# Optimization experiments

Hardware: AMD Instinct MI355X
Metric: run time of the kernel (lower is better)

The kernel has to match this reference:

```python
import jax, jax.numpy as jnp
import numpy as np


def _fft_upsample2(x):
    """Ideal (sinc) 2x upsample via FFT zero-padding, with Nyquist-bin splitting.
    x: [B, C, H, W] real -> [B, C, 2H, 2W] real."""
    H, W = x.shape[-2], x.shape[-1]
    hh, hw = H // 2, W // 2
    # shifted spectrum: index i along length-H axis <-> frequency i - H/2
    X = jnp.fft.fftshift(jnp.fft.fft2(x), axes=(-2, -1))
    Y = jnp.zeros(x.shape[:-2] + (2 * H, 2 * W), X.dtype)
    Y = Y.at[..., hh:hh + H, hw:hw + W].set(X)
    # split Nyquist row -H/2 (index hh) into +/-H/2 (indices hh and hh+H), each half
    Y = Y.at[..., hh, :].multiply(0.5)
    Y = Y.at[..., hh + H, :].set(Y[..., hh, :])
    # same for Nyquist column
    Y = Y.at[..., :, hw].multiply(0.5)
    Y = Y.at[..., :, hw + W].set(Y[..., :, hw])
    y = jnp.fft.ifft2(jnp.fft.ifftshift(Y, axes=(-2, -1))).real
    return (y * 4.0).astype(x.dtype)  # up**2 amplitude correction


def _lpf_rect_1d(N, cutoff):
    # create_lpf_rect from alias_free_convnets: ideal rect LPF in frequency
    cl = int(N * cutoff) // 2
    ch = N - cl
    rect = np.ones(N, dtype=np.float32)
    rect[cl + 1:ch] = 0.0
    if N % 4 == 0:  # half-weight on the exact cutoff (Nyquist-of-subband) bins
        rect[cl] = 0.5
        rect[ch] = 0.5
    return rect


def _lpf_rfft(x, cutoff=0.5):
    """Ideal low-pass via rfft2 with rectangular separable mask."""
    H, W = x.shape[-2], x.shape[-1]
    rect_h = _lpf_rect_1d(H, cutoff)
    rect_w = _lpf_rect_1d(W, cutoff)
    mask = jnp.asarray(rect_h[:, None] * rect_w[None, :W // 2 + 1])
    X = jnp.fft.rfft2(x) * mask
    return jnp.fft.irfft2(X, s=(H, W)).astype(x.dtype)


def setup_inputs() -> dict:
    key = jax.random.key(0)
    x = jax.random.normal(key, (8, 256, 64, 64), dtype=jnp.float32)
    return {"x": x}


def reference(x):
    u = _fft_upsample2(x)          # [B, C, 2H, 2W]
    a = jax.nn.silu(u)
    f = _lpf_rfft(a, cutoff=0.5)   # [B, C, 2H, 2W]
    return f[:, :, ::2, ::2]       # [B, C, H, W]
```

## Files before the change

kernel.cpp:

```cpp
#include <hip/hip_runtime.h>
#include <math.h>

#define TPB 256

typedef _Float16 f16x8 __attribute__((ext_vector_type(8)));
typedef float    f32x4 __attribute__((ext_vector_type(4)));

#define MFMA16(A, B, C) __builtin_amdgcn_mfma_f32_16x16x32_f16((A), (B), (C), 0, 0, 0)


__device__ __forceinline__ void store4h(_Float16* p, float a0, float a1, float a2, float a3) {
  float2 q;
  q.x = __builtin_bit_cast(float, __builtin_amdgcn_cvt_pkrtz(a0, a1));
  q.y = __builtin_bit_cast(float, __builtin_amdgcn_cvt_pkrtz(a2, a3));
  *(float2*)p = q;
}

__global__ __launch_bounds__(TPB, 3) void warped_mfma(const float* __restrict__ xin,
                                                      float* __restrict__ outp, int nimg) {
  constexpr int SA = 72;
  constexpr int SB = 136;
  constexpr int SZ = 68;

  __shared__ __attribute__((aligned(16))) unsigned char bufA[128 * SB * 2];
  __shared__ __attribute__((aligned(16))) unsigned char bufB[128 * SA * 2];
  __shared__ float k1d[128];

  _Float16* const buf0 = (_Float16*)bufA;
  _Float16* const buf2 = (_Float16*)bufA;
  float*    const buf4 = (float*)bufA;
  _Float16* const buf1 = (_Float16*)bufB;
  _Float16* const buf3 = (_Float16*)bufB;

  const int tid = threadIdx.x;
  const int lane = tid & 63;
  const int w  = tid >> 6;
  const int wk = w >> 1;
  const int wd = w & 1;
  const int lq = lane >> 4;
  const int ln = lane & 15;

  if (tid < 128) {
    const int d = tid;
    float s = 1.0f + ((d & 1) ? 0.0f : ((d & 2) ? -1.0f : 1.0f));
    for (int f = 1; f <= 31; ++f) {
      int r = (f * d) & 127;
      s += 2.0f * __cosf((float)r * 0.04908738521234052f );
    }
    k1d[d] = s * (1.0f / 64.0f);
  }
  __syncthreads();

  f16x8 AK[4][2];
#pragma unroll
  for (int t = 0; t < 4; ++t)
#pragma unroll
    for (int ks = 0; ks < 2; ++ks) {
      const int a = (wk * 4 + t) * 16 + ln;
      f16x8 f;
#pragma unroll
      for (int j = 0; j < 8; ++j) {
        int k = ks * 32 + lq * 8 + j;
        f[j] = (_Float16)k1d[(a - 2 * k) & 127];
      }
      AK[t][ks] = f;
    }
  f16x8 BT[2][4];
#pragma unroll
  for (int t = 0; t < 2; ++t)
#pragma unroll
    for (int ks = 0; ks < 4; ++ks) {
      const int c = (wk * 2 + t) * 16 + ln;
      f16x8 f;
#pragma unroll
      for (int j = 0; j < 8; ++j) {
        int k = ks * 32 + lq * 8 + j;
        f[j] = (_Float16)k1d[(k - 2 * c) & 127];
      }
      BT[t][ks] = f;
    }

  const f32x4 vzero = {0.0f, 0.0f, 0.0f, 0.0f};

  for (int img = blockIdx.x; img < nimg; img += gridDim.x) {
    const float* __restrict__ x = xin + (size_t)img * 4096;
    float* __restrict__ out     = outp + (size_t)img * 4096;

#pragma unroll
    for (int rep = 0; rep < 4; ++rep) {
      int idx = rep * 256 + tid;
      float4 v = ((const float4*)x)[idx];
      int i = idx >> 4, j0 = (idx & 15) << 2;
      store4h(buf0 + i * SA + j0, v.x, v.y, v.z, v.w);
    }
    __syncthreads();

    {
      f32x4 acc[2][4];
#pragma unroll
      for (int mtl = 0; mtl < 2; ++mtl)
#pragma unroll
        for (int ntl = 0; ntl < 4; ++ntl) acc[mtl][ntl] = vzero;
#pragma unroll
      for (int ks = 0; ks < 2; ++ks) {
        f16x8 Ad[2];
#pragma unroll
        for (int mtl = 0; mtl < 2; ++mtl)
          Ad[mtl] = *(const f16x8*)(buf0 + ((wd * 2 + mtl) * 16 + ln) * SA + ks * 32 + lq * 8);
#pragma unroll
        for (int mtl = 0; mtl < 2; ++mtl)
#pragma unroll
          for (int ntl = 0; ntl < 4; ++ntl)
            acc[mtl][ntl] = MFMA16(Ad[mtl], AK[ntl][ks], acc[mtl][ntl]);
      }
#pragma unroll
      for (int mtl = 0; mtl < 2; ++mtl)
#pragma unroll
        for (int ntl = 0; ntl < 4; ++ntl) {
          int n0 = (wk * 4 + ntl) * 16, m0 = (wd * 2 + mtl) * 16;
          f32x4 a = acc[mtl][ntl];
          store4h(buf1 + (n0 + ln) * SA + m0 + lq * 4, a[0], a[1], a[2], a[3]);
        }
    }
    __syncthreads();

#pragma unroll
    for (int nh = 0; nh < 2; ++nh) {
      f32x4 acc[4][2];
#pragma unroll
      for (int mtl = 0; mtl < 4; ++mtl)
#pragma unroll
        for (int ntl = 0; ntl < 2; ++ntl) acc[mtl][ntl] = vzero;
#pragma unroll
      for (int ks = 0; ks < 2; ++ks) {
        f16x8 Bd[2];
#pragma unroll
        for (int ntl = 0; ntl < 2; ++ntl)
          Bd[ntl] =
              *(const f16x8*)(buf1 + ((wd * 4 + nh * 2 + ntl) * 16 + ln) * SA + ks * 32 + lq * 8);
#pragma unroll
        for (int mtl = 0; mtl < 4; ++mtl)
#pragma unroll
          for (int ntl = 0; ntl < 2; ++ntl)
            acc[mtl][ntl] = MFMA16(AK[mtl][ks], Bd[ntl], acc[mtl][ntl]);
      }
#pragma unroll
      for (int mtl = 0; mtl < 4; ++mtl)
#pragma unroll
        for (int ntl = 0; ntl < 2; ++ntl) {
          int n0 = (wd * 4 + nh * 2 + ntl) * 16, m0 = (wk * 4 + mtl) * 16;
          float s[4];
#pragma unroll
          for (int r = 0; r < 4; ++r) {
            float u = acc[mtl][ntl][r];
            s[r] = u * __builtin_amdgcn_rcpf(1.0f + __expf(-u));
          }
          store4h(buf2 + (n0 + ln) * SB + m0 + lq * 4, s[0], s[1], s[2], s[3]);
        }
    }
    __syncthreads();

    {
      f32x4 acc[4][2];
#pragma unroll
      for (int mtl = 0; mtl < 4; ++mtl)
#pragma unroll
        for (int ntl = 0; ntl < 2; ++ntl) acc[mtl][ntl] = vzero;
#pragma unroll
      for (int ks = 0; ks < 4; ++ks) {
        f16x8 Ad[4];
#pragma unroll
        for (int mtl = 0; mtl < 4; ++mtl)
          Ad[mtl] = *(const f16x8*)(buf2 + ((wd * 4 + mtl) * 16 + ln) * SB + ks * 32 + lq * 8);
#pragma unroll
        for (int mtl = 0; mtl < 4; ++mtl)
#pragma unroll
          for (int ntl = 0; ntl < 2; ++ntl)
            acc[mtl][ntl] = MFMA16(Ad[mtl], BT[ntl][ks], acc[mtl][ntl]);
      }
#pragma unroll
      for (int mtl = 0; mtl < 4; ++mtl)
#pragma unroll
        for (int ntl = 0; ntl < 2; ++ntl) {
          int n0 = (wk * 2 + ntl) * 16, m0 = (wd * 4 + mtl) * 16;
          f32x4 a = acc[mtl][ntl];
          store4h(buf3 + (n0 + ln) * SB + m0 + lq * 4, a[0], a[1], a[2], a[3]);
        }
    }
    __syncthreads();

    {
      f32x4 acc[2][2];
#pragma unroll
      for (int mtl = 0; mtl < 2; ++mtl)
#pragma unroll
        for (int ntl = 0; ntl < 2; ++ntl) acc[mtl][ntl] = vzero;
#pragma unroll
      for (int ks = 0; ks < 4; ++ks) {
        f16x8 Ad[2];
#pragma unroll
        for (int mtl = 0; mtl < 2; ++mtl)
          Ad[mtl] = *(const f16x8*)(buf3 + ((wd * 2 + mtl) * 16 + ln) * SB + ks * 32 + lq * 8);
#pragma unroll
        for (int mtl = 0; mtl < 2; ++mtl)
#pragma unroll
          for (int ntl = 0; ntl < 2; ++ntl)
            acc[mtl][ntl] = MFMA16(Ad[mtl], BT[ntl][ks], acc[mtl][ntl]);
      }
#pragma unroll
      for (int mtl = 0; mtl < 2; ++mtl)
#pragma unroll
        for (int ntl = 0; ntl < 2; ++ntl) {
          int n0 = (wk * 2 + ntl) * 16, m0 = (wd * 2 + mtl) * 16;
          f32x4 o = acc[mtl][ntl];
          o[0] *= 0.25f; o[1] *= 0.25f; o[2] *= 0.25f; o[3] *= 0.25f;
          *(f32x4*)(buf4 + (n0 + ln) * SZ + m0 + lq * 4) = o;
        }
    }
    __syncthreads();

#pragma unroll
    for (int rep = 0; rep < 4; ++rep) {
      int a = (tid >> 4) + rep * 16;
      int b0 = (tid & 15) << 2;
      float4 o;
      o.x = buf4[(b0 + 0) * SZ + a];
      o.y = buf4[(b0 + 1) * SZ + a];
      o.z = buf4[(b0 + 2) * SZ + a];
      o.w = buf4[(b0 + 3) * SZ + a];
      ((float4*)out)[(a * 64 + b0) >> 2] = o;
    }
    __syncthreads();
  }
}

extern "C" void kernel_launch(void* const* d_in, const int* in_sizes, int n_in,
                              void* d_out, int out_size, void* d_ws, size_t ws_size,
                              hipStream_t stream) {
  const float* x = (const float*)d_in[0];
  float* out = (float*)d_out;
  const int nimg = in_sizes[0] / 4096;
  const int grid = (nimg + 1) / 2;
  warped_mfma<<<dim3(grid), dim3(TPB), 0, stream>>>(x, out, nimg);
}
```

Baseline: 96.54 us.

## Swizzle LDS tiles instead of padding and store output directly from MFMA accumulators

Replaces the padded LDS row strides with XOR-swizzled addressing for the 64- and 128-wide fp16 tiles, which avoids bank conflicts without padding and shrinks the LDS footprint. It also drops the final fp32 LDS transpose stage and its two barriers, writing the scaled accumulators straight to global memory. The cost is scalar, less coalesced global stores (16 contiguous floats per row segment) in place of float4 stores.

New measurement: 116.1 us. 20.3% more time.

```diff
diff --git a/kernel.cpp b/kernel.cpp
--- a/kernel.cpp
+++ b/kernel.cpp
@@ -8,6 +8,13 @@
 
 #define MFMA16(A, B, C) __builtin_amdgcn_mfma_f32_16x16x32_f16((A), (B), (C), 0, 0, 0)
 
+
+__device__ __forceinline__ int sw64(int r, int c) {
+  return (r << 6) + (c & 7) + ((((c >> 3) ^ r) & 7) << 3);
+}
+__device__ __forceinline__ int sw128(int r, int c) {
+  return (r << 7) + (c & 7) + ((((c >> 3) ^ (r & 7))) << 3);
+}
 
 __device__ __forceinline__ void store4h(_Float16* p, float a0, float a1, float a2, float a3) {
   float2 q;
@@ -18,19 +25,14 @@
 
 __global__ __launch_bounds__(TPB, 3) void warped_mfma(const float* __restrict__ xin,
                                                       float* __restrict__ outp, int nimg) {
-  constexpr int SA = 72;
-  constexpr int SB = 136;
-  constexpr int SZ = 68;
-
-  __shared__ __attribute__((aligned(16))) unsigned char bufA[128 * SB * 2];
-  __shared__ __attribute__((aligned(16))) unsigned char bufB[128 * SA * 2];
+  __shared__ __attribute__((aligned(16))) _Float16 bufA[128 * 128];
+  __shared__ __attribute__((aligned(16))) _Float16 bufB[128 * 64];
   __shared__ float k1d[128];
 
-  _Float16* const buf0 = (_Float16*)bufA;
-  _Float16* const buf2 = (_Float16*)bufA;
-  float*    const buf4 = (float*)bufA;
-  _Float16* const buf1 = (_Float16*)bufB;
-  _Float16* const buf3 = (_Float16*)bufB;
+  _Float16* const buf0 = bufA;
+  _Float16* const buf2 = bufA;
+  _Float16* const buf1 = bufB;
+  _Float16* const buf3 = bufB;
 
   const int tid = threadIdx.x;
   const int lane = tid & 63;
@@ -91,7 +93,7 @@
       int idx = rep * 256 + tid;
       float4 v = ((const float4*)x)[idx];
       int i = idx >> 4, j0 = (idx & 15) << 2;
-      store4h(buf0 + i * SA + j0, v.x, v.y, v.z, v.w);
+      store4h(buf0 + sw64(i, j0), v.x, v.y, v.z, v.w);
     }
     __syncthreads();
 
@@ -106,7 +108,7 @@
         f16x8 Ad[2];
 #pragma unroll
         for (int mtl = 0; mtl < 2; ++mtl)
-          Ad[mtl] = *(const f16x8*)(buf0 + ((wd * 2 + mtl) * 16 + ln) * SA + ks * 32 + lq * 8);
+          Ad[mtl] = *(const f16x8*)(buf0 + sw64((wd * 2 + mtl) * 16 + ln, ks * 32 + lq * 8));
 #pragma unroll
         for (int mtl = 0; mtl < 2; ++mtl)
 #pragma unroll
@@ -119,7 +121,7 @@
         for (int ntl = 0; ntl < 4; ++ntl) {
           int n0 = (wk * 4 + ntl) * 16, m0 = (wd * 2 + mtl) * 16;
           f32x4 a = acc[mtl][ntl];
-          store4h(buf1 + (n0 + ln) * SA + m0 + lq * 4, a[0], a[1], a[2], a[3]);
+          store4h(buf1 + sw64(n0 + ln, m0 + lq * 4), a[0], a[1], a[2], a[3]);
         }
     }
     __syncthreads();
@@ -136,8 +138,8 @@
         f16x8 Bd[2];
 #pragma unroll
         for (int ntl = 0; ntl < 2; ++ntl)
-          Bd[ntl] =
-              *(const f16x8*)(buf1 + ((wd * 4 + nh * 2 + ntl) * 16 + ln) * SA + ks * 32 + lq * 8);
+          Bd[ntl] = *(const f16x8*)(buf1 +
+                                    sw64((wd * 4 + nh * 2 + ntl) * 16 + ln, ks * 32 + lq * 8));
 #pragma unroll
         for (int mtl = 0; mtl < 4; ++mtl)
 #pragma unroll
@@ -155,7 +157,7 @@
             float u = acc[mtl][ntl][r];
             s[r] = u * __builtin_amdgcn_rcpf(1.0f + __expf(-u));
           }
-          store4h(buf2 + (n0 + ln) * SB + m0 + lq * 4, s[0], s[1], s[2], s[3]);
+          store4h(buf2 + sw128(n0 + ln, m0 + lq * 4), s[0], s[1], s[2], s[3]);
         }
     }
     __syncthreads();
@@ -171,7 +173,7 @@
         f16x8 Ad[4];
 #pragma unroll
         for (int mtl = 0; mtl < 4; ++mtl)
-          Ad[mtl] = *(const f16x8*)(buf2 + ((wd * 4 + mtl) * 16 + ln) * SB + ks * 32 + lq * 8);
+          Ad[mtl] = *(const f16x8*)(buf2 + sw128((wd * 4 + mtl) * 16 + ln, ks * 32 + lq * 8));
 #pragma unroll
         for (int mtl = 0; mtl < 4; ++mtl)
 #pragma unroll
@@ -184,7 +186,7 @@
         for (int ntl = 0; ntl < 2; ++ntl) {
           int n0 = (wk * 2 + ntl) * 16, m0 = (wd * 4 + mtl) * 16;
           f32x4 a = acc[mtl][ntl];
-          store4h(buf3 + (n0 + ln) * SB + m0 + lq * 4, a[0], a[1], a[2], a[3]);
+          store4h(buf3 + sw128(n0 + ln, m0 + lq * 4), a[0], a[1], a[2], a[3]);
         }
     }
     __syncthreads();
@@ -200,7 +202,7 @@
         f16x8 Ad[2];
 #pragma unroll
         for (int mtl = 0; mtl < 2; ++mtl)
-          Ad[mtl] = *(const f16x8*)(buf3 + ((wd * 2 + mtl) * 16 + ln) * SB + ks * 32 + lq * 8);
+          Ad[mtl] = *(const f16x8*)(buf3 + sw128((wd * 2 + mtl) * 16 + ln, ks * 32 + lq * 8));
 #pragma unroll
         for (int mtl = 0; mtl < 2; ++mtl)
 #pragma unroll
@@ -212,25 +214,11 @@
 #pragma unroll
         for (int ntl = 0; ntl < 2; ++ntl) {
           int n0 = (wk * 2 + ntl) * 16, m0 = (wd * 2 + mtl) * 16;
-          f32x4 o = acc[mtl][ntl];
-          o[0] *= 0.25f; o[1] *= 0.25f; o[2] *= 0.25f; o[3] *= 0.25f;
-          *(f32x4*)(buf4 + (n0 + ln) * SZ + m0 + lq * 4) = o;
-        }
-    }
-    __syncthreads();
-
-#pragma unroll
-    for (int rep = 0; rep < 4; ++rep) {
-      int a = (tid >> 4) + rep * 16;
-      int b0 = (tid & 15) << 2;
-      float4 o;
-      o.x = buf4[(b0 + 0) * SZ + a];
-      o.y = buf4[(b0 + 1) * SZ + a];
-      o.z = buf4[(b0 + 2) * SZ + a];
-      o.w = buf4[(b0 + 3) * SZ + a];
-      ((float4*)out)[(a * 64 + b0) >> 2] = o;
-    }
-    __syncthreads();
+#pragma unroll
+          for (int r = 0; r < 4; ++r)
+            out[(m0 + lq * 4 + r) * 64 + n0 + ln] = 0.25f * acc[mtl][ntl][r];
+        }
+    }
   }
 }
 
```
